# Performance work log

Hardware: AMD Instinct MI355X
Metric: run time of the kernel (lower is better)

The kernel has to match this reference:

```python
import jax, jax.numpy as jnp
import numpy as np

WS = 8            # window_size
SHIFT = WS // 2   # shift_size


def _relative_position_index(ws):
    coords = np.stack(np.meshgrid(np.arange(ws), np.arange(ws), indexing='ij'))  # (2, ws, ws)
    coords = coords.reshape(2, -1)                        # (2, ws^2)
    rel = coords[:, :, None] - coords[:, None, :]          # (2, ws^2, ws^2)
    rel = rel.transpose(1, 2, 0)
    rel[:, :, 0] += ws - 1
    rel[:, :, 1] += ws - 1
    rel[:, :, 0] *= 2 * ws - 1
    return rel.sum(-1).astype(np.int32)                   # (ws^2, ws^2)


def _shift_mask(H, W, ws, shift):
    # Swin-style region-id mask for shifted windows -> bool (nh, nw, ws^2, ws^2)
    img = np.zeros((H, W), dtype=np.int32)
    cnt = 0
    sl = (slice(0, -ws), slice(-ws, -shift), slice(-shift, None))
    for hs in sl:
        for wsl in sl:
            img[hs, wsl] = cnt
            cnt += 1
    nh, nw = H // ws, W // ws
    win = img.reshape(nh, ws, nw, ws).transpose(0, 2, 1, 3).reshape(nh, nw, ws * ws)
    return win[:, :, :, None] != win[:, :, None, :]


def setup_inputs() -> dict:
    key = jax.random.key(0)
    ks = jax.random.split(key, 6)
    B, H, W, D, NHEAD = 8, 256, 256, 96, 6
    x = jax.random.normal(ks[0], (B, H, W, D), dtype=jnp.float32)
    w_qkv = jax.random.normal(ks[1], (D, 3 * D), dtype=jnp.float32) * 0.05
    b_qkv = jnp.zeros((3 * D,), dtype=jnp.float32)
    w_out = jax.random.normal(ks[2], (D, D), dtype=jnp.float32) * 0.05
    b_out = jnp.zeros((D,), dtype=jnp.float32)
    rpe_table = jax.random.normal(ks[3], ((2 * WS - 1) ** 2, NHEAD), dtype=jnp.float32) * 0.02
    rp_index = jnp.asarray(_relative_position_index(WS))
    mask = jnp.asarray(_shift_mask(H, W, WS, SHIFT))
    return {"x": x, "w_qkv": w_qkv, "b_qkv": b_qkv, "w_out": w_out,
            "b_out": b_out, "rpe_table": rpe_table, "rp_index": rp_index, "mask": mask}


def _partition(t, ws):
    # (B, h, H, W, dk) -> (B, h, nh, nw, ws*ws, dk)
    B, h, H, W, dk = t.shape
    nh, nw = H // ws, W // ws
    t = t.reshape(B, h, nh, ws, nw, ws, dk).transpose(0, 1, 2, 4, 3, 5, 6)
    return t.reshape(B, h, nh, nw, ws * ws, dk)


def _merge(t, ws):
    # inverse of _partition -> (B, h, H, W, dk)
    B, h, nh, nw, _, dk = t.shape
    t = t.reshape(B, h, nh, nw, ws, ws, dk).transpose(0, 1, 2, 4, 3, 5, 6)
    return t.reshape(B, h, nh * ws, nw * ws, dk)


def reference(x, w_qkv, b_qkv, w_out, b_out, rpe_table, rp_index, mask):
    B, H, W, D = x.shape
    n_head = rpe_table.shape[1]
    d_k = D // n_head
    scale = 1.0 / np.sqrt(d_k)
    ws2 = mask.shape[-1]
    ws = int(round(ws2 ** 0.5))
    shift = ws // 2

    qkv = (x @ w_qkv + b_qkv).reshape(B, H, W, 3, n_head, d_k)
    qkv = qkv.transpose(3, 0, 4, 1, 2, 5)          # (3, B, h, H, W, dk)
    q, k, v = qkv[0], qkv[1], qkv[2]

    # cyclic shift
    q = jnp.roll(q, (-shift, -shift), axis=(2, 3))
    k = jnp.roll(k, (-shift, -shift), axis=(2, 3))
    v = jnp.roll(v, (-shift, -shift), axis=(2, 3))

    q = _partition(q, ws)                          # (B, h, nh, nw, ws^2, dk)
    k = _partition(k, ws)
    v = _partition(v, ws)

    scores = jnp.einsum('bhijqd,bhijkd->bhijqk', q, k) * scale
    bias = rpe_table[rp_index]                     # (ws^2, ws^2, h)
    scores = scores + bias.transpose(2, 0, 1)[None, :, None, None]
    scores = jnp.where(mask[None, None], -1e9, scores)
    attn = jax.nn.softmax(scores, axis=-1)

    out = jnp.einsum('bhijqk,bhijkd->bhijqd', attn, v)
    out = _merge(out, ws)                          # (B, h, H, W, dk)
    out = jnp.roll(out, (shift, shift), axis=(2, 3))
    out = out.transpose(0, 2, 3, 1, 4).reshape(B, H, W, D)
    return out @ w_out + b_out
```

## Files before the change

### kernel.cpp

```cpp
#include <hip/hip_runtime.h>
#include <stdint.h>

#define HH    256
#define DD    96
#define NH    6
#define WSZ   8

typedef __bf16 bf16_t;
typedef bf16_t bf16x8 __attribute__((ext_vector_type(8)));
typedef short  s16x4  __attribute__((ext_vector_type(4)));
typedef float  f32x4  __attribute__((ext_vector_type(4)));

union U2  { bf16_t h[2]; uint32_t u; };
union Upk { uint32_t u[2]; s16x4 s; };

#define LOG2E 1.44269504088896f

static __device__ __forceinline__ uint32_t pack2(float a, float b) {
    U2 x; x.h[0] = (bf16_t)a; x.h[1] = (bf16_t)b; return x.u;
}

static __device__ __forceinline__ f32x4 mfma16(s16x4 a, s16x4 b, f32x4 c) {
#if __has_builtin(__builtin_amdgcn_mfma_f32_16x16x16bf16_1k)
    return __builtin_amdgcn_mfma_f32_16x16x16bf16_1k(a, b, c, 0, 0, 0);
#else
    f32x4 d;
    asm volatile("v_mfma_f32_16x16x16_bf16 %0, %1, %2, %3"
                 : "=v"(d) : "v"(a), "v"(b), "v"(c));
    return d;
#endif
}

static __device__ __forceinline__ float fast_exp2(float x) {
#if __has_builtin(__builtin_amdgcn_exp2f)
    return __builtin_amdgcn_exp2f(x);
#else
    return exp2f(x);
#endif
}

static __device__ __forceinline__ float fast_rcp(float x) {
#if __has_builtin(__builtin_amdgcn_rcpf)
    return __builtin_amdgcn_rcpf(x);
#else
    return 1.0f / x;
#endif
}

#define OFF_WQT_HI 0
#define OFF_WQT_LO 36864
#define OFF_WV_HI  73728
#define OFF_WV_LO  92160
#define OFF_WO_HI  110592
#define OFF_WO_LO  129024
#define OFF_RPE    147456

static __device__ __forceinline__ int swz(int row, int col) {
    return row * 128 + ((((col >> 3) ^ (row & 15)) & 15) << 3) + (col & 7);
}

__global__ __launch_bounds__(256)
void prep_kernel(const float* __restrict__ wqkv, const float* __restrict__ wout,
                 const float* __restrict__ rpe, char* __restrict__ ws)
{
    bf16_t* wqt_hi = (bf16_t*)(ws + OFF_WQT_HI);
    bf16_t* wqt_lo = (bf16_t*)(ws + OFF_WQT_LO);
    bf16_t* wv_hi  = (bf16_t*)(ws + OFF_WV_HI);
    bf16_t* wv_lo  = (bf16_t*)(ws + OFF_WV_LO);
    bf16_t* wo_hi  = (bf16_t*)(ws + OFF_WO_HI);
    bf16_t* wo_lo  = (bf16_t*)(ws + OFF_WO_LO);
    float*  rpe_b  = (float*)(ws + OFF_RPE);

    int idx = blockIdx.x * 256 + threadIdx.x;
    {
        int j = idx & 7, lane = (idx >> 3) & 63, frag = idx >> 9;
        int c = lane & 15, g = lane >> 4;
        if (idx < 18432) {
            int ks = frag % 3, r2 = frag / 3, wh = r2 % 6, t = r2 / 6;
            int k = ks * 32 + g * 8 + j;
            float v = wqkv[k * 288 + t * 96 + wh * 16 + c];
            bf16_t h = (bf16_t)v;
            wqt_hi[idx] = h;
            wqt_lo[idx] = (bf16_t)(v - (float)h);
        }
        if (idx < 9216) {
            int ks = frag % 3, wh = frag / 3;
            int k = ks * 32 + g * 8 + j;
            float v = wqkv[k * 288 + 192 + wh * 16 + c];
            bf16_t h = (bf16_t)v;
            wv_hi[idx] = h;
            wv_lo[idx] = (bf16_t)(v - (float)h);
            float v2 = wout[k * 96 + wh * 16 + c];
            bf16_t h2 = (bf16_t)v2;
            wo_hi[idx] = h2;
            wo_lo[idx] = (bf16_t)(v2 - (float)h2);
        }
    }
    if (idx < 24576) {
        int i = idx & 3, lane = (idx >> 2) & 63, kt = (idx >> 8) & 3,
            nt = (idx >> 10) & 3, h = idx >> 12;
        int c = lane & 15, g = lane >> 4;
        int k = kt * 16 + g * 4 + i, q = nt * 16 + c;
        int qr = q >> 3, qc = q & 7, kr = k >> 3, kc = k & 7;
        rpe_b[idx] = rpe[((qr - kr + 7) * 15 + (qc - kc + 7)) * NH + h] * LOG2E;
    }
}

__global__ __launch_bounds__(768, 4)
void swin_mfma(const float* __restrict__ x,
               const float* __restrict__ b_qkv,
               const float* __restrict__ b_out,
               const char*  __restrict__ ws,
               float* __restrict__ out)
{
    __shared__ char smem[32768];

    const int tid  = threadIdx.x;
    const int w2   = tid >> 6;
    const int wv   = (w2 >= 6) ? 1 : 0;
    const int w    = w2 - 6 * wv;
    const int lane = tid & 63;
    const int g    = lane >> 4;
    const int c    = lane & 15;
    const int tl   = tid - (wv << 8) - (wv << 7);

    bf16_t* xs_hi = (bf16_t*)(smem + (wv << 14));
    bf16_t* o_hi  = xs_hi;

    const bf16_t* wqt_hi = (const bf16_t*)(ws + OFF_WQT_HI);
    const bf16_t* wqt_lo = (const bf16_t*)(ws + OFF_WQT_LO);
    const bf16_t* wv_hi  = (const bf16_t*)(ws + OFF_WV_HI);
    const bf16_t* wv_lo  = (const bf16_t*)(ws + OFF_WV_LO);
    const bf16_t* wo_hi  = (const bf16_t*)(ws + OFF_WO_HI);
    const bf16_t* wo_lo  = (const bf16_t*)(ws + OFF_WO_LO);
    const float*  rpe_b  = (const float*)(ws + OFF_RPE);

    const int blk = blockIdx.x;
    const int b   = blk >> 9;
    const int wi  = (blk >> 4) & 31;
    const int wj  = ((blk & 15) << 1) + wv;

    const f32x4 zf = {0.f, 0.f, 0.f, 0.f};

    #pragma unroll
    for (int it = 0; it < 4; ++it) {
        int f4  = tl + it * 384;
        int row = f4 / 24, c4 = f4 - row * 24;
        int r = row >> 3, cl = row & 7;
        int gh = (wi * WSZ + r + 4) & 255;
        int gw = (wj * WSZ + cl + 4) & 255;
        const float4 v = *(const float4*)(x + (((size_t)b * HH + gh) * HH + gw) * DD + c4 * 4);
        uint2 hv;
        hv.x = pack2(v.x, v.y); hv.y = pack2(v.z, v.w);
        *(uint2*)&xs_hi[swz(row, c4 * 4)] = hv;
    }
    __syncthreads();

    f32x4 aq[4], akk[4], av[4];
    {
        const float4 bq4 = *(const float4*)&b_qkv[w * 16 + 4 * g];
        const float4 bk4 = *(const float4*)&b_qkv[96 + w * 16 + 4 * g];
        const float  bv  = b_qkv[192 + w * 16 + c];
        #pragma unroll
        for (int t4 = 0; t4 < 4; ++t4) {
            aq[t4]  = (f32x4){bq4.x, bq4.y, bq4.z, bq4.w};
            akk[t4] = (f32x4){bk4.x, bk4.y, bk4.z, bk4.w};
            av[t4]  = (f32x4){bv, bv, bv, bv};
        }
    }
    #pragma unroll
    for (int ks = 0; ks < 3; ++ks) {
        bf16x8 ah[4];
        #pragma unroll
        for (int mt = 0; mt < 4; ++mt) {
            int e = (mt * 16 + c) * 128 + (((ks * 4 + g) ^ c) << 3);
            ah[mt] = *(const bf16x8*)&xs_hi[e];
        }
        const bf16x8 qh = *(const bf16x8*)&wqt_hi[(w * 3 + ks) * 512 + lane * 8];
        const bf16x8 ql = *(const bf16x8*)&wqt_lo[(w * 3 + ks) * 512 + lane * 8];
        const bf16x8 kh = *(const bf16x8*)&wqt_hi[((6 + w) * 3 + ks) * 512 + lane * 8];
        const bf16x8 kl = *(const bf16x8*)&wqt_lo[((6 + w) * 3 + ks) * 512 + lane * 8];
        const bf16x8 vh = *(const bf16x8*)&wv_hi[(w * 3 + ks) * 512 + lane * 8];
        const bf16x8 vl = *(const bf16x8*)&wv_lo[(w * 3 + ks) * 512 + lane * 8];
        #pragma unroll
        for (int mt = 0; mt < 4; ++mt) {
            aq[mt]  = __builtin_amdgcn_mfma_f32_16x16x32_bf16(qh, ah[mt], aq[mt], 0, 0, 0);
            aq[mt]  = __builtin_amdgcn_mfma_f32_16x16x32_bf16(ql, ah[mt], aq[mt], 0, 0, 0);
            akk[mt] = __builtin_amdgcn_mfma_f32_16x16x32_bf16(kh, ah[mt], akk[mt], 0, 0, 0);
            akk[mt] = __builtin_amdgcn_mfma_f32_16x16x32_bf16(kl, ah[mt], akk[mt], 0, 0, 0);
            av[mt]  = __builtin_amdgcn_mfma_f32_16x16x32_bf16(ah[mt], vh, av[mt], 0, 0, 0);
            av[mt]  = __builtin_amdgcn_mfma_f32_16x16x32_bf16(ah[mt], vl, av[mt], 0, 0, 0);
        }
    }
    __syncthreads();

    s16x4 aqb[4], akb[4], avb[4];
    #pragma unroll
    for (int t = 0; t < 4; ++t) {
        Upk uq, uk, uv;
        const float qs = 0.25f * LOG2E;
        uq.u[0] = pack2(aq[t][0] * qs, aq[t][1] * qs);
        uq.u[1] = pack2(aq[t][2] * qs, aq[t][3] * qs);
        uk.u[0] = pack2(akk[t][0], akk[t][1]);
        uk.u[1] = pack2(akk[t][2], akk[t][3]);
        uv.u[0] = pack2(av[t][0], av[t][1]);
        uv.u[1] = pack2(av[t][2], av[t][3]);
        aqb[t] = uq.s; akb[t] = uk.s; avb[t] = uv.s;
    }

    const int e_wi = (wi == 31), e_wj = (wj == 31);
    const bool edge = e_wi || e_wj;
    int rk[4][4];
    #pragma unroll
    for (int kt = 0; kt < 4; ++kt)
        #pragma unroll
        for (int i = 0; i < 4; ++i) {
            int k = kt * 16 + g * 4 + i;
            int kr = k >> 3, kc = k & 7;
            rk[kt][i] = (e_wi ? (kr >= 4 ? 2 : 1) : 0) * 3 + (e_wj ? (kc >= 4 ? 2 : 1) : 0);
        }

    #pragma unroll
    for (int nt = 0; nt < 4; ++nt) {
        f32x4 stc[4];
        #pragma unroll
        for (int kt = 0; kt < 4; ++kt) {
            const f32x4 rc = *(const f32x4*)&rpe_b[(((w * 4 + nt) * 4 + kt) << 8) + lane * 4];
            stc[kt] = mfma16(akb[kt], aqb[nt], rc);
        }

        int q = nt * 16 + c, qr = q >> 3, qc = q & 7;
        int rq = (e_wi ? (qr >= 4 ? 2 : 1) : 0) * 3 + (e_wj ? (qc >= 4 ? 2 : 1) : 0);
        float sv[16];
        float sum = 0.f;
        #pragma unroll
        for (int kt = 0; kt < 4; ++kt)
            #pragma unroll
            for (int i = 0; i < 4; ++i) {
                float s = stc[kt][i];
                if (edge && (rk[kt][i] != rq)) s = -1e9f;
                s = fast_exp2(s);
                sv[kt * 4 + i] = s;
                sum += s;
            }
        sum += __shfl_xor(sum, 16);
        sum += __shfl_xor(sum, 32);
        const float rinv = fast_rcp(sum);

        f32x4 oa = zf;
        #pragma unroll
        for (int ks2 = 0; ks2 < 4; ++ks2) {
            Upk pb;
            pb.u[0] = pack2(sv[ks2 * 4 + 0], sv[ks2 * 4 + 1]);
            pb.u[1] = pack2(sv[ks2 * 4 + 2], sv[ks2 * 4 + 3]);
            oa = mfma16(avb[ks2], pb.s, oa);
        }
        {
            uint2 hv;
            hv.x = pack2(oa[0] * rinv, oa[1] * rinv);
            hv.y = pack2(oa[2] * rinv, oa[3] * rinv);
            *(uint2*)&o_hi[swz(nt * 16 + c, w * 16 + 4 * g)] = hv;
        }
    }
    __syncthreads();

    f32x4 acc3[4];
    {
        const float boc = b_out[w * 16 + c];
        #pragma unroll
        for (int mt = 0; mt < 4; ++mt) acc3[mt] = (f32x4){boc, boc, boc, boc};
    }
    #pragma unroll
    for (int ks = 0; ks < 3; ++ks) {
        bf16x8 ah[4];
        #pragma unroll
        for (int mt = 0; mt < 4; ++mt) {
            int e = (mt * 16 + c) * 128 + (((ks * 4 + g) ^ c) << 3);
            ah[mt] = *(const bf16x8*)&o_hi[e];
        }
        const bf16x8 bh = *(const bf16x8*)&wo_hi[(w * 3 + ks) * 512 + lane * 8];
        const bf16x8 bl = *(const bf16x8*)&wo_lo[(w * 3 + ks) * 512 + lane * 8];
        #pragma unroll
        for (int mt = 0; mt < 4; ++mt) {
            acc3[mt] = __builtin_amdgcn_mfma_f32_16x16x32_bf16(ah[mt], bh, acc3[mt], 0, 0, 0);
            acc3[mt] = __builtin_amdgcn_mfma_f32_16x16x32_bf16(ah[mt], bl, acc3[mt], 0, 0, 0);
        }
    }
    #pragma unroll
    for (int mt = 0; mt < 4; ++mt)
        #pragma unroll
        for (int i = 0; i < 4; ++i) {
            int row = mt * 16 + g * 4 + i;
            int r = row >> 3, cl = row & 7;
            int gh = (wi * WSZ + r + 4) & 255;
            int gw = (wj * WSZ + cl + 4) & 255;
            out[(((size_t)b * HH + gh) * HH + gw) * DD + w * 16 + c] = acc3[mt][i];
        }
}

extern "C" void kernel_launch(void* const* d_in, const int* in_sizes, int n_in,
                              void* d_out, int out_size, void* d_ws, size_t ws_size,
                              hipStream_t stream) {
    const float* x    = (const float*)d_in[0];
    const float* wqkv = (const float*)d_in[1];
    const float* bqkv = (const float*)d_in[2];
    const float* wout = (const float*)d_in[3];
    const float* bout = (const float*)d_in[4];
    const float* rpe  = (const float*)d_in[5];
    float* out = (float*)d_out;
    char* ws = (char*)d_ws;

    const int B = in_sizes[0] / (HH * HH * DD);

    hipLaunchKernelGGL(prep_kernel, dim3(96), dim3(256), 0, stream, wqkv, wout, rpe, ws);
    hipLaunchKernelGGL(swin_mfma, dim3(B * 512), dim3(768), 0, stream,
                       x, bqkv, bout, (const char*)ws, out);
}
```

Baseline: 186.6 us.

## Load x fragments directly from global into MFMA registers and vectorize output stores

Removes the LDS staging of the input window: each lane now reads its fp32 x fragment straight from global memory, converts it to bf16 and feeds the QKV MFMAs, which drops one LDS round trip and two barriers. The output projection swaps operand order so each lane holds four consecutive channels of one pixel, allowing a single 16-byte store per tile instead of scalar strided stores. Per-pixel global addresses are precomputed once. The trade-off is that x is now read redundantly by all six head waves instead of once per block, relying on L1/L2 to absorb it.

```diff
diff --git a/kernel.cpp b/kernel.cpp
--- a/kernel.cpp
+++ b/kernel.cpp
@@ -12,6 +12,7 @@
 typedef float  f32x4  __attribute__((ext_vector_type(4)));
 
 union U2  { bf16_t h[2]; uint32_t u; };
+union U4  { bf16x8 v; uint32_t u[4]; };
 union Upk { uint32_t u[2]; s16x4 s; };
 
 #define LOG2E 1.44269504088896f
@@ -122,10 +123,8 @@
     const int lane = tid & 63;
     const int g    = lane >> 4;
     const int c    = lane & 15;
-    const int tl   = tid - (wv << 8) - (wv << 7);
-
-    bf16_t* xs_hi = (bf16_t*)(smem + (wv << 14));
-    bf16_t* o_hi  = xs_hi;
+
+    bf16_t* o_hi = (bf16_t*)(smem + (wv << 14));
 
     const bf16_t* wqt_hi = (const bf16_t*)(ws + OFF_WQT_HI);
     const bf16_t* wqt_lo = (const bf16_t*)(ws + OFF_WQT_LO);
@@ -140,21 +139,16 @@
     const int wi  = (blk >> 4) & 31;
     const int wj  = ((blk & 15) << 1) + wv;
 
+    uint32_t pix[4];
+    #pragma unroll
+    for (int t = 0; t < 4; ++t) {
+        int p = t * 16 + c;
+        int gh = (wi * WSZ + (p >> 3) + 4) & 255;
+        int gw = (wj * WSZ + (p & 7) + 4) & 255;
+        pix[t] = (((uint32_t)b * HH + gh) << 8) + gw;
+    }
+
     const f32x4 zf = {0.f, 0.f, 0.f, 0.f};
-
-    #pragma unroll
-    for (int it = 0; it < 4; ++it) {
-        int f4  = tl + it * 384;
-        int row = f4 / 24, c4 = f4 - row * 24;
-        int r = row >> 3, cl = row & 7;
-        int gh = (wi * WSZ + r + 4) & 255;
-        int gw = (wj * WSZ + cl + 4) & 255;
-        const float4 v = *(const float4*)(x + (((size_t)b * HH + gh) * HH + gw) * DD + c4 * 4);
-        uint2 hv;
-        hv.x = pack2(v.x, v.y); hv.y = pack2(v.z, v.w);
-        *(uint2*)&xs_hi[swz(row, c4 * 4)] = hv;
-    }
-    __syncthreads();
 
     f32x4 aq[4], akk[4], av[4];
     {
@@ -173,8 +167,13 @@
         bf16x8 ah[4];
         #pragma unroll
         for (int mt = 0; mt < 4; ++mt) {
-            int e = (mt * 16 + c) * 128 + (((ks * 4 + g) ^ c) << 3);
-            ah[mt] = *(const bf16x8*)&xs_hi[e];
+            const float* xp = x + (size_t)pix[mt] * DD + ks * 32 + g * 8;
+            const float4 lo = *(const float4*)xp;
+            const float4 hi = *(const float4*)(xp + 4);
+            U4 u;
+            u.u[0] = pack2(lo.x, lo.y); u.u[1] = pack2(lo.z, lo.w);
+            u.u[2] = pack2(hi.x, hi.y); u.u[3] = pack2(hi.z, hi.w);
+            ah[mt] = u.v;
         }
         const bf16x8 qh = *(const bf16x8*)&wqt_hi[(w * 3 + ks) * 512 + lane * 8];
         const bf16x8 ql = *(const bf16x8*)&wqt_lo[(w * 3 + ks) * 512 + lane * 8];
@@ -192,7 +191,6 @@
             av[mt]  = __builtin_amdgcn_mfma_f32_16x16x32_bf16(ah[mt], vl, av[mt], 0, 0, 0);
         }
     }
-    __syncthreads();
 
     s16x4 aqb[4], akb[4], avb[4];
     #pragma unroll
@@ -266,36 +264,30 @@
 
     f32x4 acc3[4];
     {
-        const float boc = b_out[w * 16 + c];
-        #pragma unroll
-        for (int mt = 0; mt < 4; ++mt) acc3[mt] = (f32x4){boc, boc, boc, boc};
+        const float4 bo4 = *(const float4*)&b_out[w * 16 + 4 * g];
+        #pragma unroll
+        for (int nt = 0; nt < 4; ++nt)
+            acc3[nt] = (f32x4){bo4.x, bo4.y, bo4.z, bo4.w};
     }
     #pragma unroll
     for (int ks = 0; ks < 3; ++ks) {
-        bf16x8 ah[4];
-        #pragma unroll
-        for (int mt = 0; mt < 4; ++mt) {
-            int e = (mt * 16 + c) * 128 + (((ks * 4 + g) ^ c) << 3);
-            ah[mt] = *(const bf16x8*)&o_hi[e];
+        bf16x8 oh[4];
+        #pragma unroll
+        for (int nt = 0; nt < 4; ++nt) {
+            int e = (nt * 16 + c) * 128 + (((ks * 4 + g) ^ c) << 3);
+            oh[nt] = *(const bf16x8*)&o_hi[e];
         }
         const bf16x8 bh = *(const bf16x8*)&wo_hi[(w * 3 + ks) * 512 + lane * 8];
         const bf16x8 bl = *(const bf16x8*)&wo_lo[(w * 3 + ks) * 512 + lane * 8];
         #pragma unroll
-        for (int mt = 0; mt < 4; ++mt) {
-            acc3[mt] = __builtin_amdgcn_mfma_f32_16x16x32_bf16(ah[mt], bh, acc3[mt], 0, 0, 0);
-            acc3[mt] = __builtin_amdgcn_mfma_f32_16x16x32_bf16(ah[mt], bl, acc3[mt], 0, 0, 0);
-        }
-    }
-    #pragma unroll
-    for (int mt = 0; mt < 4; ++mt)
-        #pragma unroll
-        for (int i = 0; i < 4; ++i) {
-            int row = mt * 16 + g * 4 + i;
-            int r = row >> 3, cl = row & 7;
-            int gh = (wi * WSZ + r + 4) & 255;
-            int gw = (wj * WSZ + cl + 4) & 255;
-            out[(((size_t)b * HH + gh) * HH + gw) * DD + w * 16 + c] = acc3[mt][i];
-        }
+        for (int nt = 0; nt < 4; ++nt) {
+            acc3[nt] = __builtin_amdgcn_mfma_f32_16x16x32_bf16(bh, oh[nt], acc3[nt], 0, 0, 0);
+            acc3[nt] = __builtin_amdgcn_mfma_f32_16x16x32_bf16(bl, oh[nt], acc3[nt], 0, 0, 0);
+        }
+    }
+    #pragma unroll
+    for (int nt = 0; nt < 4; ++nt)
+        *(f32x4*)(out + (size_t)pix[nt] * DD + w * 16 + 4 * g) = acc3[nt];
 }
 
 extern "C" void kernel_launch(void* const* d_in, const int* in_sizes, int n_in,
```

Result: slower. 285.8 us (+53.2%).
